# Kernel optimization log

Hardware: AMD Instinct MI355X
Metric: run time of the kernel (lower is better)

Reference implementation:

```python
import jax, jax.numpy as jnp
import numpy as np

DIM = 768
N_HEADS = 12
HEAD_DIM = DIM // N_HEADS
B, T = 2, 2048


def setup_inputs() -> dict:
    key = jax.random.key(0)
    ks = jax.random.split(key, 11)
    s = 0.02
    return {
        "q_in": jax.random.normal(ks[0], (B, T, DIM), jnp.float32),
        "k_in": jax.random.normal(ks[1], (B, T, DIM), jnp.float32),
        "v_in": jax.random.normal(ks[2], (B, T, DIM), jnp.float32),
        "Wq": jax.random.normal(ks[3], (DIM, DIM), jnp.float32) * s,
        "bq": jnp.zeros((DIM,), jnp.float32),
        "Wk": jax.random.normal(ks[4], (DIM, DIM), jnp.float32) * s,
        "bk": jnp.zeros((DIM,), jnp.float32),
        "Wv": jax.random.normal(ks[5], (DIM, DIM), jnp.float32) * s,
        "bv": jnp.zeros((DIM,), jnp.float32),
        "Wo": jax.random.normal(ks[6], (DIM, DIM), jnp.float32) * s,
        "bo": jnp.zeros((DIM,), jnp.float32),
    }


def reference(q_in, k_in, v_in, Wq, bq, Wk, bk, Wv, bv, Wo, bo):
    b, t, c = q_in.shape
    scale = HEAD_DIM ** -0.5
    # linear projections (torch Linear: x @ W.T + b)
    q = q_in @ Wq.T + bq
    k = k_in @ Wk.T + bk
    v = v_in @ Wv.T + bv
    # [b, t, h, d] -> [b, h, t, d]
    q = q.reshape(b, t, N_HEADS, HEAD_DIM).transpose(0, 2, 1, 3)
    k = k.reshape(b, t, N_HEADS, HEAD_DIM).transpose(0, 2, 1, 3)
    v = v.reshape(b, t, N_HEADS, HEAD_DIM).transpose(0, 2, 1, 3)
    scores = jnp.einsum("bhqd,bhkd->bhqk", q, k) * scale  # full TxT scores
    probs = jax.nn.softmax(scores, axis=-1)
    attn = jnp.einsum("bhqk,bhkd->bhqd", probs, v)
    attn = attn.transpose(0, 2, 1, 3).reshape(b, t, c)
    return attn @ Wo.T + bo
```

## Files before the change

kernel.cpp:

```cpp
#include <hip/hip_runtime.h>


typedef unsigned short u16;
typedef __attribute__((ext_vector_type(8))) short short8;
typedef __attribute__((ext_vector_type(4))) float float4v;

#define DIMC 768
#define NTOK 4096
#define NHD  12
#define HDD  64
#define SEQT 2048

__device__ __forceinline__ u16 f2bf(float f) {
  union { float f; unsigned u; } v; v.f = f;
  unsigned r = v.u + 0x7fffu + ((v.u >> 16) & 1u);
  return (u16)(r >> 16);
}
__device__ __forceinline__ float bf2f(u16 u) {
  union { unsigned u; float f; } v; v.u = ((unsigned)u) << 16;
  return v.f;
}

__global__ __launch_bounds__(256) void cvt_all(
    const float* __restrict__ a0, const float* __restrict__ a1, const float* __restrict__ a2,
    const float* __restrict__ a3, const float* __restrict__ a4, const float* __restrict__ a5,
    const float* __restrict__ a6,
    u16* __restrict__ o0, u16* __restrict__ o1, u16* __restrict__ o2,
    u16* __restrict__ o3, u16* __restrict__ o4, u16* __restrict__ o5,
    u16* __restrict__ o6) {
  int bid = blockIdx.x;
  const float* s; u16* d; int inner;
  if (bid < 9216) {
    int z = bid / 3072; inner = bid - z * 3072;
    s = (z == 0) ? a0 : (z == 1) ? a1 : a2;
    d = (z == 0) ? o0 : (z == 1) ? o1 : o2;
  } else {
    int r = bid - 9216; int z = r / 576; inner = r - z * 576;
    s = (z == 0) ? a3 : (z == 1) ? a4 : (z == 2) ? a5 : a6;
    d = (z == 0) ? o3 : (z == 1) ? o4 : (z == 2) ? o5 : o6;
  }
  size_t i = ((size_t)inner * 256 + threadIdx.x) * 4;
  float4 v = *(const float4*)(s + i);
  *(ushort4*)(d + i) = make_ushort4(f2bf(v.x), f2bf(v.y), f2bf(v.z), f2bf(v.w));
}

__device__ __forceinline__ void gemm_mainloop3(
    const u16* __restrict__ X, const u16* __restrict__ W,
    int m0, int n0, u16* Als, u16* Bls, float4v acc[4][4]) {
  int tid = threadIdx.x;
  int sr = tid >> 3, sc = (tid & 7) * 8;
  int w = tid >> 6, lane = tid & 63, quad = lane >> 4, r15 = lane & 15;
  int wm = (w >> 1) * 64, wn = (w & 1) * 64;
  const u16* xp0 = X + (size_t)(m0 + sr) * DIMC + sc;
  const u16* xp1 = xp0 + 32 * DIMC;
  const u16* xp2 = xp0 + 64 * DIMC;
  const u16* xp3 = xp0 + 96 * DIMC;
  const u16* wp0 = W + (size_t)(n0 + sr) * DIMC + sc;
  const u16* wp1 = wp0 + 32 * DIMC;
  const u16* wp2 = wp0 + 64 * DIMC;
  const u16* wp3 = wp0 + 96 * DIMC;
  uint4 pa0 = *(const uint4*)xp0, pa1 = *(const uint4*)xp1;
  uint4 pa2 = *(const uint4*)xp2, pa3 = *(const uint4*)xp3;
  uint4 pb0 = *(const uint4*)wp0, pb1 = *(const uint4*)wp1;
  uint4 pb2 = *(const uint4*)wp2, pb3 = *(const uint4*)wp3;
  for (int k0 = 0; k0 < DIMC; k0 += 64) {
    __syncthreads();
    *(uint4*)(Als + sr * 72 + sc) = pa0;
    *(uint4*)(Als + (sr + 32) * 72 + sc) = pa1;
    *(uint4*)(Als + (sr + 64) * 72 + sc) = pa2;
    *(uint4*)(Als + (sr + 96) * 72 + sc) = pa3;
    *(uint4*)(Bls + sr * 72 + sc) = pb0;
    *(uint4*)(Bls + (sr + 32) * 72 + sc) = pb1;
    *(uint4*)(Bls + (sr + 64) * 72 + sc) = pb2;
    *(uint4*)(Bls + (sr + 96) * 72 + sc) = pb3;
    __syncthreads();
    int kn = k0 + 64;
    if (kn < DIMC) {
      pa0 = *(const uint4*)(xp0 + kn); pa1 = *(const uint4*)(xp1 + kn);
      pa2 = *(const uint4*)(xp2 + kn); pa3 = *(const uint4*)(xp3 + kn);
      pb0 = *(const uint4*)(wp0 + kn); pb1 = *(const uint4*)(wp1 + kn);
      pb2 = *(const uint4*)(wp2 + kn); pb3 = *(const uint4*)(wp3 + kn);
    }
    #pragma unroll
    for (int sk = 0; sk < 2; sk++) {
      short8 af[4], bf[4];
      #pragma unroll
      for (int mf = 0; mf < 4; mf++)
        af[mf] = *(const short8*)(Als + (wm + mf * 16 + r15) * 72 + sk * 32 + quad * 8);
      #pragma unroll
      for (int nf = 0; nf < 4; nf++)
        bf[nf] = *(const short8*)(Bls + (wn + nf * 16 + r15) * 72 + sk * 32 + quad * 8);
      #pragma unroll
      for (int mf = 0; mf < 4; mf++)
        #pragma unroll
        for (int nf = 0; nf < 4; nf++)
          acc[mf][nf] = __builtin_amdgcn_mfma_f32_16x16x32_bf16(af[mf], bf[nf], acc[mf][nf], 0, 0, 0);
    }
  }
}

__global__ __launch_bounds__(256, 2) void gemm_qkv(
    const u16* __restrict__ xq, const u16* __restrict__ xk, const u16* __restrict__ xv,
    const u16* __restrict__ wq, const u16* __restrict__ wk, const u16* __restrict__ wv,
    const float* __restrict__ bq, const float* __restrict__ bk, const float* __restrict__ bv,
    u16* __restrict__ Qh, u16* __restrict__ Kh, u16* __restrict__ Vt) {
  __shared__ __align__(16) u16 LS[2 * 128 * 72];
  u16* Als = LS;
  u16* Bls = LS + 128 * 72;
  int z = blockIdx.z;
  const u16* X = (z == 0) ? xq : (z == 1) ? xk : xv;
  const u16* W = (z == 0) ? wq : (z == 1) ? wk : wv;
  const float* bias = (z == 0) ? bq : (z == 1) ? bk : bv;
  int m0 = blockIdx.x * 128, n0 = blockIdx.y * 128;
  float4v acc[4][4];
  #pragma unroll
  for (int i = 0; i < 4; i++)
    #pragma unroll
    for (int j = 0; j < 4; j++)
      #pragma unroll
      for (int r = 0; r < 4; r++) acc[i][j][r] = 0.f;
  gemm_mainloop3(X, W, m0, n0, Als, Bls, acc);
  int tid = threadIdx.x, w = tid >> 6, lane = tid & 63, quad = lane >> 4, r15 = lane & 15;
  int wm = (w >> 1) * 64, wn = (w & 1) * 64;
  if (z == 2) {
    __syncthreads();
    u16* T = LS;
    #pragma unroll
    for (int mf = 0; mf < 4; mf++)
      #pragma unroll
      for (int nf = 0; nf < 4; nf++)
        #pragma unroll
        for (int rg = 0; rg < 4; rg++) {
          int mloc = wm + mf * 16 + quad * 4 + rg;
          int nloc = wn + nf * 16 + r15;
          T[nloc * 136 + mloc] = f2bf(acc[mf][nf][rg] + bias[n0 + nloc]);
        }
    __syncthreads();
    int r = tid >> 1, seg = tid & 1;
    int b = m0 >> 11, t0 = m0 & 2047;
    int h = (n0 + r) >> 6, d = (n0 + r) & 63;
    size_t base = (((size_t)(b * NHD + h)) * HDD + d) * SEQT + t0 + seg * 64;
    const u16* src = T + r * 136 + seg * 64;
    #pragma unroll
    for (int j = 0; j < 8; j++)
      *(uint4*)(Vt + base + j * 8) = *(const uint4*)(src + j * 8);
  } else {
    #pragma unroll
    for (int mf = 0; mf < 4; mf++)
      #pragma unroll
      for (int nf = 0; nf < 4; nf++)
        #pragma unroll
        for (int rg = 0; rg < 4; rg++) {
          int m = m0 + wm + mf * 16 + quad * 4 + rg;
          int n = n0 + wn + nf * 16 + r15;
          float val = acc[mf][nf][rg] + bias[n];
          if (z == 0) val *= 0.180336880f;
          int b = m >> 11, t = m & 2047, h = n >> 6, d = n & 63;
          u16 o = f2bf(val);
          size_t bh = (size_t)(b * NHD + h);
          if (z == 0) Qh[(bh * SEQT + t) * HDD + d] = o;
          else Kh[(bh * SEQT + t) * HDD + d] = o;
        }
  }
}

__global__ __launch_bounds__(256, 4) void attn_kernel(
    const u16* __restrict__ Qh, const u16* __restrict__ Kh, const u16* __restrict__ Vt,
    u16* __restrict__ Opart, float* __restrict__ Lpart) {
  __shared__ __align__(16) u16 Kls[64 * 64];
  __shared__ __align__(16) u16 Vls[64 * 64];
  __shared__ __align__(16) u16 Pls[4 * 32 * 64];
  int bh = blockIdx.y, sp = blockIdx.z, qt0 = blockIdx.x * 128;
  int tid = threadIdx.x, w = tid >> 6, lane = tid & 63, quad = lane >> 4, r15 = lane & 15;
  int qw = qt0 + w * 32;
  const int nt = 8;
  int kt0 = sp * (nt * 64);

  int rr = r15 & 7;
  int sx0 = (quad ^ rr) * 8;
  int sx1 = ((4 + quad) ^ rr) * 8;

  short8 qa[2][2];
  #pragma unroll
  for (int qs = 0; qs < 2; qs++) {
    const u16* qp = Qh + ((size_t)bh * SEQT + qw + qs * 16 + r15) * HDD + quad * 8;
    qa[qs][0] = *(const short8*)qp;
    qa[qs][1] = *(const short8*)(qp + 32);
  }
  float4v fzero;
  #pragma unroll
  for (int r = 0; r < 4; r++) fzero[r] = 0.f;

  float4v oacc[2][4];
  float lsum[2];
  #pragma unroll
  for (int qs = 0; qs < 2; qs++) {
    lsum[qs] = 0.f;
    #pragma unroll
    for (int dt = 0; dt < 4; dt++)
      #pragma unroll
      for (int r = 0; r < 4; r++) oacc[qs][dt][r] = 0.f;
  }

  const u16* Kbase = Kh + (size_t)bh * SEQT * HDD;
  const u16* Vbase = Vt + (size_t)bh * HDD * SEQT;
  u16* Pw = Pls + w * (32 * 64);
  int sr = tid >> 3, sc = (tid & 7) * 8;
  int sg = (((tid & 7) ^ (sr & 7)) * 8);

  uint4 pk0 = *(const uint4*)(Kbase + (size_t)(kt0 + sr) * HDD + sc);
  uint4 pk1 = *(const uint4*)(Kbase + (size_t)(kt0 + sr + 32) * HDD + sc);
  uint4 pv0 = *(const uint4*)(Vbase + (size_t)sr * SEQT + kt0 + sc);
  uint4 pv1 = *(const uint4*)(Vbase + (size_t)(sr + 32) * SEQT + kt0 + sc);

  for (int it = 0; it < nt; it++) {
    __syncthreads();
    *(uint4*)(Kls + sr * 64 + sg) = pk0;
    *(uint4*)(Kls + (sr + 32) * 64 + sg) = pk1;
    *(uint4*)(Vls + sr * 64 + sg) = pv0;
    *(uint4*)(Vls + (sr + 32) * 64 + sg) = pv1;
    __syncthreads();
    int nit = it + 1; if (nit == nt) nit = 0;
    int ktn = kt0 + nit * 64;
    pk0 = *(const uint4*)(Kbase + (size_t)(ktn + sr) * HDD + sc);
    pk1 = *(const uint4*)(Kbase + (size_t)(ktn + sr + 32) * HDD + sc);
    pv0 = *(const uint4*)(Vbase + (size_t)sr * SEQT + ktn + sc);
    pv1 = *(const uint4*)(Vbase + (size_t)(sr + 32) * SEQT + ktn + sc);

    __builtin_amdgcn_s_setprio(1);
    #pragma unroll
    for (int nk = 0; nk < 4; nk++) {
      short8 k0 = *(const short8*)(Kls + (nk * 16 + r15) * 64 + sx0);
      short8 k1 = *(const short8*)(Kls + (nk * 16 + r15) * 64 + sx1);
      #pragma unroll
      for (int qs = 0; qs < 2; qs++) {
        float4v zv = __builtin_amdgcn_mfma_f32_16x16x32_bf16(k0, qa[qs][0], fzero, 0, 0, 0);
        zv = __builtin_amdgcn_mfma_f32_16x16x32_bf16(k1, qa[qs][1], zv, 0, 0, 0);
        float p0 = __builtin_amdgcn_exp2f(zv[0]);
        float p1 = __builtin_amdgcn_exp2f(zv[1]);
        float p2 = __builtin_amdgcn_exp2f(zv[2]);
        float p3 = __builtin_amdgcn_exp2f(zv[3]);
        lsum[qs] += (p0 + p1) + (p2 + p3);
        unsigned lo = __builtin_amdgcn_perm(__float_as_uint(p1), __float_as_uint(p0), 0x07060302u);
        unsigned hi = __builtin_amdgcn_perm(__float_as_uint(p3), __float_as_uint(p2), 0x07060302u);
        *(uint2*)(Pw + (qs * 16 + r15) * 64 + (((nk * 4 + quad) ^ (rr << 1)) << 2)) =
            make_uint2(lo, hi);
      }
    }
    short8 pa[2][2];
    #pragma unroll
    for (int qs = 0; qs < 2; qs++) {
      pa[qs][0] = *(const short8*)(Pw + (qs * 16 + r15) * 64 + sx0);
      pa[qs][1] = *(const short8*)(Pw + (qs * 16 + r15) * 64 + sx1);
    }
    #pragma unroll
    for (int dt = 0; dt < 4; dt++) {
      short8 v0 = *(const short8*)(Vls + (dt * 16 + r15) * 64 + sx0);
      short8 v1 = *(const short8*)(Vls + (dt * 16 + r15) * 64 + sx1);
      #pragma unroll
      for (int qs = 0; qs < 2; qs++) {
        oacc[qs][dt] = __builtin_amdgcn_mfma_f32_16x16x32_bf16(pa[qs][0], v0, oacc[qs][dt], 0, 0, 0);
        oacc[qs][dt] = __builtin_amdgcn_mfma_f32_16x16x32_bf16(pa[qs][1], v1, oacc[qs][dt], 0, 0, 0);
      }
    }
    __builtin_amdgcn_s_setprio(0);
  }
  size_t obase = ((size_t)sp * 2 * NHD + bh) * SEQT;
  #pragma unroll
  for (int qs = 0; qs < 2; qs++)
    #pragma unroll
    for (int rg = 0; rg < 4; rg++) {
      int q = qw + qs * 16 + quad * 4 + rg;
      u16* orow = Opart + (obase + q) * HDD;
      #pragma unroll
      for (int dt = 0; dt < 4; dt++) orow[dt * 16 + r15] = f2bf(oacc[qs][dt][rg]);
    }
  #pragma unroll
  for (int qs = 0; qs < 2; qs++) {
    float s = lsum[qs];
    s += __shfl_xor(s, 16, 64);
    s += __shfl_xor(s, 32, 64);
    if (quad == 0) Lpart[obase + qw + qs * 16 + r15] = s;
  }
}

__global__ __launch_bounds__(256) void merge_kernel(
    const u16* __restrict__ Opart, const float* __restrict__ Lpart, u16* __restrict__ X2) {
  const size_t NXe = (size_t)2 * NHD * SEQT * HDD;
  const size_t LS = (size_t)2 * NHD * SEQT;
  int tid = threadIdx.x;
  int row = blockIdx.x * 32 + (tid >> 3);
  int dcol = (tid & 7) * 8;
  int bh = row >> 11, t = row & 2047;
  size_t off = (size_t)row * HDD + dcol;
  float inv = 1.0f / (Lpart[row] + Lpart[row + LS] +
                      Lpart[row + 2 * LS] + Lpart[row + 3 * LS]);
  int b = bh / NHD, h = bh % NHD;
  u16 o[8];
  #pragma unroll
  for (int half = 0; half < 2; half++) {
    ushort4 a = *(const ushort4*)(Opart + off + half * 4);
    ushort4 c = *(const ushort4*)(Opart + off + NXe + half * 4);
    ushort4 e = *(const ushort4*)(Opart + off + 2 * NXe + half * 4);
    ushort4 g = *(const ushort4*)(Opart + off + 3 * NXe + half * 4);
    o[half * 4 + 0] = f2bf((bf2f(a.x) + bf2f(c.x) + bf2f(e.x) + bf2f(g.x)) * inv);
    o[half * 4 + 1] = f2bf((bf2f(a.y) + bf2f(c.y) + bf2f(e.y) + bf2f(g.y)) * inv);
    o[half * 4 + 2] = f2bf((bf2f(a.z) + bf2f(c.z) + bf2f(e.z) + bf2f(g.z)) * inv);
    o[half * 4 + 3] = f2bf((bf2f(a.w) + bf2f(c.w) + bf2f(e.w) + bf2f(g.w)) * inv);
  }
  *(uint4*)(X2 + ((size_t)b * SEQT + t) * DIMC + h * HDD + dcol) = *(uint4*)o;
}

__global__ __launch_bounds__(256, 2) void gemm_out(
    const u16* __restrict__ X2, const u16* __restrict__ wo,
    const float* __restrict__ bo, float* __restrict__ out) {
  __shared__ __align__(16) u16 LS[2 * 128 * 72];
  u16* Als = LS;
  u16* Bls = LS + 128 * 72;
  int m0 = blockIdx.x * 128, n0 = blockIdx.y * 128;
  float4v acc[4][4];
  #pragma unroll
  for (int i = 0; i < 4; i++)
    #pragma unroll
    for (int j = 0; j < 4; j++)
      #pragma unroll
      for (int r = 0; r < 4; r++) acc[i][j][r] = 0.f;
  gemm_mainloop3(X2, wo, m0, n0, Als, Bls, acc);
  int tid = threadIdx.x, w = tid >> 6, lane = tid & 63, quad = lane >> 4, r15 = lane & 15;
  int wm = (w >> 1) * 64, wn = (w & 1) * 64;
  #pragma unroll
  for (int mf = 0; mf < 4; mf++)
    #pragma unroll
    for (int nf = 0; nf < 4; nf++)
      #pragma unroll
      for (int rg = 0; rg < 4; rg++) {
        int m = m0 + wm + mf * 16 + quad * 4 + rg;
        int n = n0 + wn + nf * 16 + r15;
        out[(size_t)m * DIMC + n] = acc[mf][nf][rg] + bo[n];
      }
}

extern "C" void kernel_launch(void* const* d_in, const int* in_sizes, int n_in,
                              void* d_out, int out_size, void* d_ws, size_t ws_size,
                              hipStream_t stream) {
  const float* q_in = (const float*)d_in[0];
  const float* k_in = (const float*)d_in[1];
  const float* v_in = (const float*)d_in[2];
  const float* Wq = (const float*)d_in[3];
  const float* bq = (const float*)d_in[4];
  const float* Wk = (const float*)d_in[5];
  const float* bk = (const float*)d_in[6];
  const float* Wv = (const float*)d_in[7];
  const float* bv = (const float*)d_in[8];
  const float* Wo = (const float*)d_in[9];
  const float* bo = (const float*)d_in[10];

  const size_t NX = (size_t)NTOK * DIMC;
  const size_t NW = (size_t)DIMC * DIMC;
  u16* ws = (u16*)d_ws;
  u16* qb = ws;
  u16* kb = qb + NX;
  u16* vb = kb + NX;
  u16* wqb = vb + NX;
  u16* wkb = wqb + NW;
  u16* wvb = wkb + NW;
  u16* wob = wvb + NW;
  u16* Qh = wob + NW;
  u16* Kh = Qh + NX;
  u16* Vt = Kh + NX;
  u16* X2 = Vt + NX;
  u16* Opart = X2 + NX;
  float* Lpart = (float*)(Opart + 4 * NX);

  cvt_all<<<dim3(11520), 256, 0, stream>>>(
      q_in, k_in, v_in, Wq, Wk, Wv, Wo, qb, kb, vb, wqb, wkb, wvb, wob);
  gemm_qkv<<<dim3(NTOK / 128, DIMC / 128, 3), 256, 0, stream>>>(
      qb, kb, vb, wqb, wkb, wvb, bq, bk, bv, Qh, Kh, Vt);
  attn_kernel<<<dim3(SEQT / 128, 2 * NHD, 4), 256, 0, stream>>>(Qh, Kh, Vt, Opart, Lpart);
  merge_kernel<<<dim3(2 * NHD * SEQT / 32), 256, 0, stream>>>(Opart, Lpart, X2);
  gemm_out<<<dim3(NTOK / 128, DIMC / 128), 256, 0, stream>>>(X2, wob, bo, (float*)d_out);
}
```

Before: 184.2 us.

## Feed softmax probabilities directly from registers into PV MFMA, skipping LDS

In the attention kernel, the exp'd score fragments now stay in registers and go straight into a 16x16x16 bf16 MFMA against V, with the operands swapped so the output is transposed. This removes the per-warp LDS round trip for P (store, then reload) and frees that shared memory. The cost is twice as many, smaller MFMAs of lower K depth, plus narrower 8-byte V reads from LDS. The output store is rewritten for the transposed accumulator layout as packed 8-byte writes. The old path remains as a fallback behind a builtin check.

```diff
diff --git a/kernel.cpp b/kernel.cpp
--- a/kernel.cpp
+++ b/kernel.cpp
@@ -3,6 +3,7 @@
 
 typedef unsigned short u16;
 typedef __attribute__((ext_vector_type(8))) short short8;
+typedef __attribute__((ext_vector_type(4))) short short4v;
 typedef __attribute__((ext_vector_type(4))) float float4v;
 
 #define DIMC 768
@@ -11,6 +12,12 @@
 #define HDD  64
 #define SEQT 2048
 
+#if __has_builtin(__builtin_amdgcn_mfma_f32_16x16x16bf16_1k)
+#define HAVE_MFMA16 1
+#else
+#define HAVE_MFMA16 0
+#endif
+
 __device__ __forceinline__ u16 f2bf(float f) {
   union { float f; unsigned u; } v; v.f = f;
   unsigned r = v.u + 0x7fffu + ((v.u >> 16) & 1u);
@@ -19,6 +26,9 @@
 __device__ __forceinline__ float bf2f(u16 u) {
   union { unsigned u; float f; } v; v.u = ((unsigned)u) << 16;
   return v.f;
+}
+__device__ __forceinline__ short4v u2s4(uint2 u) {
+  union { uint2 u; short4v s; } v; v.u = u; return v.s;
 }
 
 __global__ __launch_bounds__(256) void cvt_all(
@@ -169,7 +179,9 @@
     u16* __restrict__ Opart, float* __restrict__ Lpart) {
   __shared__ __align__(16) u16 Kls[64 * 64];
   __shared__ __align__(16) u16 Vls[64 * 64];
+#if !HAVE_MFMA16
   __shared__ __align__(16) u16 Pls[4 * 32 * 64];
+#endif
   int bh = blockIdx.y, sp = blockIdx.z, qt0 = blockIdx.x * 128;
   int tid = threadIdx.x, w = tid >> 6, lane = tid & 63, quad = lane >> 4, r15 = lane & 15;
   int qw = qt0 + w * 32;
@@ -179,6 +191,7 @@
   int rr = r15 & 7;
   int sx0 = (quad ^ rr) * 8;
   int sx1 = ((4 + quad) ^ rr) * 8;
+  int q1 = quad >> 1, q0 = quad & 1;
 
   short8 qa[2][2];
   #pragma unroll
@@ -204,7 +217,6 @@
 
   const u16* Kbase = Kh + (size_t)bh * SEQT * HDD;
   const u16* Vbase = Vt + (size_t)bh * HDD * SEQT;
-  u16* Pw = Pls + w * (32 * 64);
   int sr = tid >> 3, sc = (tid & 7) * 8;
   int sg = (((tid & 7) ^ (sr & 7)) * 8);
 
@@ -228,6 +240,35 @@
     pv1 = *(const uint4*)(Vbase + (size_t)(sr + 32) * SEQT + ktn + sc);
 
     __builtin_amdgcn_s_setprio(1);
+#if HAVE_MFMA16
+    #pragma unroll
+    for (int nk = 0; nk < 4; nk++) {
+      short8 k0 = *(const short8*)(Kls + (nk * 16 + r15) * 64 + sx0);
+      short8 k1 = *(const short8*)(Kls + (nk * 16 + r15) * 64 + sx1);
+      #pragma unroll
+      for (int qs = 0; qs < 2; qs++) {
+        float4v zv = __builtin_amdgcn_mfma_f32_16x16x32_bf16(k0, qa[qs][0], fzero, 0, 0, 0);
+        zv = __builtin_amdgcn_mfma_f32_16x16x32_bf16(k1, qa[qs][1], zv, 0, 0, 0);
+        float p0 = __builtin_amdgcn_exp2f(zv[0]);
+        float p1 = __builtin_amdgcn_exp2f(zv[1]);
+        float p2 = __builtin_amdgcn_exp2f(zv[2]);
+        float p3 = __builtin_amdgcn_exp2f(zv[3]);
+        lsum[qs] += (p0 + p1) + (p2 + p3);
+        uint2 pw = make_uint2(
+            __builtin_amdgcn_perm(__float_as_uint(p1), __float_as_uint(p0), 0x07060302u),
+            __builtin_amdgcn_perm(__float_as_uint(p3), __float_as_uint(p2), 0x07060302u));
+        short4v pb = u2s4(pw);
+        #pragma unroll
+        for (int dt = 0; dt < 4; dt++) {
+          uint2 vw = *(const uint2*)(Vls + (dt * 16 + r15) * 64 +
+                                     (((nk * 2 + q1) ^ rr) * 8) + q0 * 4);
+          oacc[qs][dt] = __builtin_amdgcn_mfma_f32_16x16x16bf16_1k(
+              u2s4(vw), pb, oacc[qs][dt], 0, 0, 0);
+        }
+      }
+    }
+#else
+    u16* Pw = Pls + w * (32 * 64);
     #pragma unroll
     for (int nk = 0; nk < 4; nk++) {
       short8 k0 = *(const short8*)(Kls + (nk * 16 + r15) * 64 + sx0);
@@ -263,24 +304,41 @@
         oacc[qs][dt] = __builtin_amdgcn_mfma_f32_16x16x32_bf16(pa[qs][1], v1, oacc[qs][dt], 0, 0, 0);
       }
     }
+#endif
     __builtin_amdgcn_s_setprio(0);
   }
-  size_t obase = ((size_t)sp * 2 * NHD + bh) * SEQT;
+  size_t obase = ((size_t)sp * 2 * NHD + bh) * SEQT + qw;
+#if HAVE_MFMA16
+  #pragma unroll
+  for (int qs = 0; qs < 2; qs++) {
+    u16* orow = Opart + (obase + qs * 16 + r15) * HDD + quad * 4;
+    #pragma unroll
+    for (int dt = 0; dt < 4; dt++) {
+      u16 c0 = f2bf(oacc[qs][dt][0]);
+      u16 c1 = f2bf(oacc[qs][dt][1]);
+      u16 c2 = f2bf(oacc[qs][dt][2]);
+      u16 c3 = f2bf(oacc[qs][dt][3]);
+      *(uint2*)(orow + dt * 16) =
+          make_uint2((unsigned)c0 | ((unsigned)c1 << 16),
+                     (unsigned)c2 | ((unsigned)c3 << 16));
+    }
+  }
+#else
   #pragma unroll
   for (int qs = 0; qs < 2; qs++)
     #pragma unroll
     for (int rg = 0; rg < 4; rg++) {
-      int q = qw + qs * 16 + quad * 4 + rg;
-      u16* orow = Opart + (obase + q) * HDD;
+      u16* orow = Opart + (obase + qs * 16 + quad * 4 + rg) * HDD;
       #pragma unroll
       for (int dt = 0; dt < 4; dt++) orow[dt * 16 + r15] = f2bf(oacc[qs][dt][rg]);
     }
+#endif
   #pragma unroll
   for (int qs = 0; qs < 2; qs++) {
     float s = lsum[qs];
     s += __shfl_xor(s, 16, 64);
     s += __shfl_xor(s, 32, 64);
-    if (quad == 0) Lpart[obase + qw + qs * 16 + r15] = s;
+    if (quad == 0) Lpart[obase + qs * 16 + r15] = s;
   }
 }
 
```

Result: slower. 189.8 us (+3.0%).

## Double-buffer K/V tiles in LDS for attention to drop one barrier per tile

Applied to the files above, without the earlier changes.

The attention kernel now keeps two LDS buffers for K and V and ping-pongs between them. The loop is fully unrolled so each tile needs one __syncthreads instead of two, and the global load for the next tile is issued before the current tile is computed. The old dummy wrap-around prefetch on the last iteration is gone. LDS per block grows by 16 KB and launch bounds drop from 4 to 3 blocks per SM, which may reduce occupancy.

```diff
diff --git a/kernel.cpp b/kernel.cpp
--- a/kernel.cpp
+++ b/kernel.cpp
@@ -164,17 +164,68 @@
   }
 }
 
-__global__ __launch_bounds__(256, 4) void attn_kernel(
+#define LOAD_TILE(kt)                                                        \
+  pk0 = *(const uint4*)(Kbase + (size_t)((kt) + sr) * HDD + sc);             \
+  pk1 = *(const uint4*)(Kbase + (size_t)((kt) + sr + 32) * HDD + sc);        \
+  pv0 = *(const uint4*)(Vbase + (size_t)sr * SEQT + (kt) + sc);              \
+  pv1 = *(const uint4*)(Vbase + (size_t)(sr + 32) * SEQT + (kt) + sc);
+
+#define STAGE_TILE(Kd, Vd)                                                   \
+  *(uint4*)((Kd) + sr * 64 + sg) = pk0;                                      \
+  *(uint4*)((Kd) + (sr + 32) * 64 + sg) = pk1;                               \
+  *(uint4*)((Vd) + sr * 64 + sg) = pv0;                                      \
+  *(uint4*)((Vd) + (sr + 32) * 64 + sg) = pv1;
+
+#define COMPUTE_TILE(Kc, Vc)                                                 \
+  {                                                                          \
+    __builtin_amdgcn_s_setprio(1);                                           \
+    _Pragma("unroll")                                                        \
+    for (int nk = 0; nk < 4; nk++) {                                         \
+      short8 k0 = *(const short8*)((Kc) + (nk * 16 + r15) * 64 + sx0);       \
+      short8 k1 = *(const short8*)((Kc) + (nk * 16 + r15) * 64 + sx1);       \
+      _Pragma("unroll")                                                      \
+      for (int qs = 0; qs < 2; qs++) {                                       \
+        float4v zv = __builtin_amdgcn_mfma_f32_16x16x32_bf16(k0, qa[qs][0], fzero, 0, 0, 0); \
+        zv = __builtin_amdgcn_mfma_f32_16x16x32_bf16(k1, qa[qs][1], zv, 0, 0, 0); \
+        float p0 = __builtin_amdgcn_exp2f(zv[0]);                            \
+        float p1 = __builtin_amdgcn_exp2f(zv[1]);                            \
+        float p2 = __builtin_amdgcn_exp2f(zv[2]);                            \
+        float p3 = __builtin_amdgcn_exp2f(zv[3]);                            \
+        lsum[qs] += (p0 + p1) + (p2 + p3);                                   \
+        unsigned lo = __builtin_amdgcn_perm(__float_as_uint(p1), __float_as_uint(p0), 0x07060302u); \
+        unsigned hi = __builtin_amdgcn_perm(__float_as_uint(p3), __float_as_uint(p2), 0x07060302u); \
+        *(uint2*)(Pw + (qs * 16 + r15) * 64 + (((nk * 4 + quad) ^ (rr << 1)) << 2)) = \
+            make_uint2(lo, hi);                                              \
+      }                                                                      \
+    }                                                                        \
+    short8 pa00 = *(const short8*)(Pw + (r15) * 64 + sx0);                   \
+    short8 pa01 = *(const short8*)(Pw + (r15) * 64 + sx1);                   \
+    short8 pa10 = *(const short8*)(Pw + (16 + r15) * 64 + sx0);              \
+    short8 pa11 = *(const short8*)(Pw + (16 + r15) * 64 + sx1);              \
+    _Pragma("unroll")                                                        \
+    for (int dt = 0; dt < 4; dt++) {                                         \
+      short8 v0 = *(const short8*)((Vc) + (dt * 16 + r15) * 64 + sx0);       \
+      short8 v1 = *(const short8*)((Vc) + (dt * 16 + r15) * 64 + sx1);       \
+      oacc[0][dt] = __builtin_amdgcn_mfma_f32_16x16x32_bf16(pa00, v0, oacc[0][dt], 0, 0, 0); \
+      oacc[0][dt] = __builtin_amdgcn_mfma_f32_16x16x32_bf16(pa01, v1, oacc[0][dt], 0, 0, 0); \
+      oacc[1][dt] = __builtin_amdgcn_mfma_f32_16x16x32_bf16(pa10, v0, oacc[1][dt], 0, 0, 0); \
+      oacc[1][dt] = __builtin_amdgcn_mfma_f32_16x16x32_bf16(pa11, v1, oacc[1][dt], 0, 0, 0); \
+    }                                                                        \
+    __builtin_amdgcn_s_setprio(0);                                           \
+  }
+
+__global__ __launch_bounds__(256, 3) void attn_kernel(
     const u16* __restrict__ Qh, const u16* __restrict__ Kh, const u16* __restrict__ Vt,
     u16* __restrict__ Opart, float* __restrict__ Lpart) {
-  __shared__ __align__(16) u16 Kls[64 * 64];
-  __shared__ __align__(16) u16 Vls[64 * 64];
+  __shared__ __align__(16) u16 K0ls[64 * 64];
+  __shared__ __align__(16) u16 V0ls[64 * 64];
+  __shared__ __align__(16) u16 K1ls[64 * 64];
+  __shared__ __align__(16) u16 V1ls[64 * 64];
   __shared__ __align__(16) u16 Pls[4 * 32 * 64];
   int bh = blockIdx.y, sp = blockIdx.z, qt0 = blockIdx.x * 128;
   int tid = threadIdx.x, w = tid >> 6, lane = tid & 63, quad = lane >> 4, r15 = lane & 15;
   int qw = qt0 + w * 32;
-  const int nt = 8;
-  int kt0 = sp * (nt * 64);
+  int kt0 = sp * 512;
 
   int rr = r15 & 7;
   int sx0 = (quad ^ rr) * 8;
@@ -208,70 +259,33 @@
   int sr = tid >> 3, sc = (tid & 7) * 8;
   int sg = (((tid & 7) ^ (sr & 7)) * 8);
 
-  uint4 pk0 = *(const uint4*)(Kbase + (size_t)(kt0 + sr) * HDD + sc);
-  uint4 pk1 = *(const uint4*)(Kbase + (size_t)(kt0 + sr + 32) * HDD + sc);
-  uint4 pv0 = *(const uint4*)(Vbase + (size_t)sr * SEQT + kt0 + sc);
-  uint4 pv1 = *(const uint4*)(Vbase + (size_t)(sr + 32) * SEQT + kt0 + sc);
-
-  for (int it = 0; it < nt; it++) {
-    __syncthreads();
-    *(uint4*)(Kls + sr * 64 + sg) = pk0;
-    *(uint4*)(Kls + (sr + 32) * 64 + sg) = pk1;
-    *(uint4*)(Vls + sr * 64 + sg) = pv0;
-    *(uint4*)(Vls + (sr + 32) * 64 + sg) = pv1;
-    __syncthreads();
-    int nit = it + 1; if (nit == nt) nit = 0;
-    int ktn = kt0 + nit * 64;
-    pk0 = *(const uint4*)(Kbase + (size_t)(ktn + sr) * HDD + sc);
-    pk1 = *(const uint4*)(Kbase + (size_t)(ktn + sr + 32) * HDD + sc);
-    pv0 = *(const uint4*)(Vbase + (size_t)sr * SEQT + ktn + sc);
-    pv1 = *(const uint4*)(Vbase + (size_t)(sr + 32) * SEQT + ktn + sc);
-
-    __builtin_amdgcn_s_setprio(1);
-    #pragma unroll
-    for (int nk = 0; nk < 4; nk++) {
-      short8 k0 = *(const short8*)(Kls + (nk * 16 + r15) * 64 + sx0);
-      short8 k1 = *(const short8*)(Kls + (nk * 16 + r15) * 64 + sx1);
-      #pragma unroll
-      for (int qs = 0; qs < 2; qs++) {
-        float4v zv = __builtin_amdgcn_mfma_f32_16x16x32_bf16(k0, qa[qs][0], fzero, 0, 0, 0);
-        zv = __builtin_amdgcn_mfma_f32_16x16x32_bf16(k1, qa[qs][1], zv, 0, 0, 0);
-        float p0 = __builtin_amdgcn_exp2f(zv[0]);
-        float p1 = __builtin_amdgcn_exp2f(zv[1]);
-        float p2 = __builtin_amdgcn_exp2f(zv[2]);
-        float p3 = __builtin_amdgcn_exp2f(zv[3]);
-        lsum[qs] += (p0 + p1) + (p2 + p3);
-        unsigned lo = __builtin_amdgcn_perm(__float_as_uint(p1), __float_as_uint(p0), 0x07060302u);
-        unsigned hi = __builtin_amdgcn_perm(__float_as_uint(p3), __float_as_uint(p2), 0x07060302u);
-        *(uint2*)(Pw + (qs * 16 + r15) * 64 + (((nk * 4 + quad) ^ (rr << 1)) << 2)) =
-            make_uint2(lo, hi);
-      }
+  uint4 pk0, pk1, pv0, pv1;
+
+  LOAD_TILE(kt0)
+  STAGE_TILE(K0ls, V0ls)
+  __syncthreads();
+  #pragma unroll
+  for (int ib = 0; ib < 4; ib++) {
+    LOAD_TILE(kt0 + (ib * 2 + 1) * 64)
+    COMPUTE_TILE(K0ls, V0ls)
+    STAGE_TILE(K1ls, V1ls)
+    __syncthreads();
+    if (ib < 3) {
+      LOAD_TILE(kt0 + (ib * 2 + 2) * 64)
+      COMPUTE_TILE(K1ls, V1ls)
+      STAGE_TILE(K0ls, V0ls)
+      __syncthreads();
+    } else {
+      COMPUTE_TILE(K1ls, V1ls)
     }
-    short8 pa[2][2];
-    #pragma unroll
-    for (int qs = 0; qs < 2; qs++) {
-      pa[qs][0] = *(const short8*)(Pw + (qs * 16 + r15) * 64 + sx0);
-      pa[qs][1] = *(const short8*)(Pw + (qs * 16 + r15) * 64 + sx1);
-    }
-    #pragma unroll
-    for (int dt = 0; dt < 4; dt++) {
-      short8 v0 = *(const short8*)(Vls + (dt * 16 + r15) * 64 + sx0);
-      short8 v1 = *(const short8*)(Vls + (dt * 16 + r15) * 64 + sx1);
-      #pragma unroll
-      for (int qs = 0; qs < 2; qs++) {
-        oacc[qs][dt] = __builtin_amdgcn_mfma_f32_16x16x32_bf16(pa[qs][0], v0, oacc[qs][dt], 0, 0, 0);
-        oacc[qs][dt] = __builtin_amdgcn_mfma_f32_16x16x32_bf16(pa[qs][1], v1, oacc[qs][dt], 0, 0, 0);
-      }
-    }
-    __builtin_amdgcn_s_setprio(0);
-  }
-  size_t obase = ((size_t)sp * 2 * NHD + bh) * SEQT;
+  }
+
+  size_t obase = ((size_t)sp * 2 * NHD + bh) * SEQT + qw;
   #pragma unroll
   for (int qs = 0; qs < 2; qs++)
     #pragma unroll
     for (int rg = 0; rg < 4; rg++) {
-      int q = qw + qs * 16 + quad * 4 + rg;
-      u16* orow = Opart + (obase + q) * HDD;
+      u16* orow = Opart + (obase + qs * 16 + quad * 4 + rg) * HDD;
       #pragma unroll
       for (int dt = 0; dt < 4; dt++) orow[dt * 16 + r15] = f2bf(oacc[qs][dt][rg]);
     }
@@ -280,7 +294,7 @@
     float s = lsum[qs];
     s += __shfl_xor(s, 16, 64);
     s += __shfl_xor(s, 32, 64);
-    if (quad == 0) Lpart[obase + qw + qs * 16 + r15] = s;
+    if (quad == 0) Lpart[obase + qs * 16 + r15] = s;
   }
 }
 
```

Result: slower. 262.2 us (+42.3%).
